# Kernel optimization log

Measured on AMD Instinct MI355X. Metric: run time of the kernel, lower is better.

## Reference

```python
import jax, jax.numpy as jnp
import numpy as np

B, N, IN_DIM, OUT_DIM, HEADS = 4, 2048, 128, 32, 8
NEG_SLOPE = 0.2


def setup_inputs() -> dict:
    key = jax.random.key(0)
    k_x, k_adj, k_w, k_as, k_ad = jax.random.split(key, 5)
    x = jax.random.normal(k_x, (B, N, IN_DIM), dtype=jnp.float32)
    adj = jax.random.randint(k_adj, (B, N, N), 0, 2).astype(jnp.float32)
    # xavier_uniform bounds
    lim_w = float(np.sqrt(6.0 / (IN_DIM + OUT_DIM)))
    lim_a = float(np.sqrt(6.0 / (OUT_DIM + 1)))
    W = jax.random.uniform(k_w, (HEADS, IN_DIM, OUT_DIM), dtype=jnp.float32, minval=-lim_w, maxval=lim_w)
    a_src = jax.random.uniform(k_as, (HEADS, OUT_DIM), dtype=jnp.float32, minval=-lim_a, maxval=lim_a)
    a_dst = jax.random.uniform(k_ad, (HEADS, OUT_DIM), dtype=jnp.float32, minval=-lim_a, maxval=lim_a)
    return {"x": x, "adj": adj, "W": W, "a_src": a_src, "a_dst": a_dst}


def reference(x, adj, W, a_src, a_dst):
    # Wh: [B,H,N,O]
    Wh = jnp.einsum('bnf,hfo->bhno', x, W)
    alpha_src = jnp.einsum('bhno,ho->bhn', Wh, a_src)  # [B,H,N]
    alpha_dst = jnp.einsum('bhno,ho->bhn', Wh, a_dst)  # [B,H,N]
    # additive scores e[b,h,i,j] = alpha_src[b,h,i] + alpha_dst[b,h,j]
    e = alpha_src[..., :, None] + alpha_dst[..., None, :]
    e = jnp.where(e >= 0, e, NEG_SLOPE * e)  # leaky_relu(0.2)
    n = adj.shape[-1]
    eye = jnp.eye(n, dtype=adj.dtype)
    mask = (adj + eye[None] > 0)[:, None, :, :]  # [B,1,N,N]
    e = jnp.where(mask, e, -jnp.inf)
    attn = jax.nn.softmax(e, axis=-1)  # every row has self-loop -> finite
    out = jnp.einsum('bhij,bhjo->bhio', attn, Wh)  # [B,H,N,O]
    b = x.shape[0]
    out = jnp.transpose(out, (0, 2, 1, 3)).reshape(b, n, HEADS * OUT_DIM)
    return jax.nn.relu(out)
```

## Files before the change

### kernel.cpp

```cpp
#include <hip/hip_runtime.h>
#include <math.h>

#define BB 4
#define NSZ 2048
#define FDIM 128
#define ODIM 32
#define HH 8

typedef short short8 __attribute__((ext_vector_type(8)));
typedef float f32x4 __attribute__((ext_vector_type(4)));

#define WS_EAP  0
#define WS_EBP  131072
#define WS_ADJB 262144
#define WS_WHF  786432
#define WS_WF   1835008

__device__ __forceinline__ unsigned bfbits(float f) {
    unsigned u = __builtin_bit_cast(unsigned, f);
    return u + 0x7fffu + ((u >> 16) & 1u);
}
__device__ __forceinline__ unsigned bfpack(float a, float b) {
    return __builtin_amdgcn_perm(bfbits(b), bfbits(a), 0x07060302);
}

__global__ __launch_bounds__(256) void k_wpack(const float* __restrict__ W,
                                               int4* __restrict__ wf) {
    int h = blockIdx.x;
    int t = threadIdx.x;
    int kt = t >> 6, lane = t & 63;
    int col = lane & 15, quad = lane >> 4;
    const float* wp = W + ((size_t)h * FDIM + kt * 32 + quad * 8) * ODIM;
#pragma unroll
    for (int ot = 0; ot < 2; ot++) {
        unsigned d[4];
#pragma unroll
        for (int jp = 0; jp < 4; jp++) {
            float lo = wp[(2 * jp) * ODIM + ot * 16 + col];
            float hi = wp[(2 * jp + 1) * ODIM + ot * 16 + col];
            d[jp] = bfpack(lo, hi);
        }
        wf[((h * 4 + kt) * 2 + ot) * 64 + lane] =
            make_int4((int)d[0], (int)d[1], (int)d[2], (int)d[3]);
    }
}

__global__ __launch_bounds__(256) void k_prep(const float* __restrict__ x,
                                              const float* __restrict__ adj,
                                              const float* __restrict__ a_src,
                                              const float* __restrict__ a_dst,
                                              const int4* __restrict__ wf,
                                              unsigned* __restrict__ adjb,
                                              int4* __restrict__ whf,
                                              float2* __restrict__ eap,
                                              float2* __restrict__ ebp) {
    __shared__ unsigned short wlds[64][33];
    int t = threadIdx.x;

    if (blockIdx.x < 16384) {
        int g = blockIdx.x * 256 + t;
        int l = g & 7;
        int word = g >> 3;
        int wk = word & 63;
        int row = word >> 6;
        int i = row & (NSZ - 1);
        const float4 v = *(const float4*)&adj[(size_t)row * NSZ + wk * 32 + l * 4];
        unsigned m = 0;
        if (v.x > 0.f) m |= 1u << (l * 4 + 0);
        if (v.y > 0.f) m |= 1u << (l * 4 + 1);
        if (v.z > 0.f) m |= 1u << (l * 4 + 2);
        if (v.w > 0.f) m |= 1u << (l * 4 + 3);
        m |= (unsigned)__shfl_xor((int)m, 1);
        m |= (unsigned)__shfl_xor((int)m, 2);
        m |= (unsigned)__shfl_xor((int)m, 4);
        if (l == 0) {
            int jb = i - wk * 32;
            if (jb >= 0 && jb < 32) m |= 1u << jb;
            adjb[word] = m;
        }
        return;
    }

    int bidx = blockIdx.x - 16384;
    int b = bidx >> 8;
    int h = (bidx >> 5) & 7;
    int nt = bidx & 31;
    int n0 = nt * 64;
    int w = t >> 6, lane = t & 63;
    int col = lane & 15, quad = lane >> 4;

    const float* xp = x + ((size_t)(b * NSZ) + n0 + w * 16 + col) * FDIM + quad * 8;
    int4 afr[4];
#pragma unroll
    for (int kt = 0; kt < 4; kt++) {
        float4 xa = *(const float4*)(xp + kt * 32);
        float4 xb = *(const float4*)(xp + kt * 32 + 4);
        afr[kt] = make_int4((int)bfpack(xa.x, xa.y), (int)bfpack(xa.z, xa.w),
                            (int)bfpack(xb.x, xb.y), (int)bfpack(xb.z, xb.w));
    }

    const int4* wfp = wf + h * 8 * 64 + lane;
    f32x4 alo = {0.f, 0.f, 0.f, 0.f};
    f32x4 ahi = {0.f, 0.f, 0.f, 0.f};
#pragma unroll
    for (int kt = 0; kt < 4; kt++) {
        short8 a8 = __builtin_bit_cast(short8, afr[kt]);
        alo = __builtin_amdgcn_mfma_f32_16x16x32_bf16(a8,
                __builtin_bit_cast(short8, wfp[(kt * 2 + 0) * 64]), alo, 0, 0, 0);
        ahi = __builtin_amdgcn_mfma_f32_16x16x32_bf16(a8,
                __builtin_bit_cast(short8, wfp[(kt * 2 + 1) * 64]), ahi, 0, 0, 0);
    }

    float as0 = a_src[h * ODIM + col], as1 = a_src[h * ODIM + 16 + col];
    float ad0 = a_dst[h * ODIM + col], ad1 = a_dst[h * ODIM + 16 + col];
#pragma unroll
    for (int r = 0; r < 4; r++) {
        float pa = alo[r] * as0 + ahi[r] * as1;
        float pb = alo[r] * ad0 + ahi[r] * ad1;
#pragma unroll
        for (int mk = 1; mk <= 8; mk <<= 1) {
            pa += __shfl_xor(pa, mk);
            pb += __shfl_xor(pb, mk);
        }
        if (col == 0) {
            size_t idx = (size_t)(b * HH + h) * NSZ + n0 + w * 16 + quad * 4 + r;
            eap[idx] = make_float2(__expf(pa - 8.f), __expf(0.2f * pa - 8.f));
            ebp[idx] = make_float2(__expf(pb - 8.f), __expf(0.2f * pb - 8.f));
        }
    }

#pragma unroll
    for (int r = 0; r < 4; r++) {
        wlds[w * 16 + quad * 4 + r][col]      = (unsigned short)(bfbits(alo[r]) >> 16);
        wlds[w * 16 + quad * 4 + r][col + 16] = (unsigned short)(bfbits(ahi[r]) >> 16);
    }
    __syncthreads();
    int jl = w >> 1, ot = w & 1;
    unsigned d[4];
#pragma unroll
    for (int jp = 0; jp < 4; jp++) {
        unsigned lo = wlds[jl * 32 + quad * 8 + 2 * jp][ot * 16 + col];
        unsigned hi = wlds[jl * 32 + quad * 8 + 2 * jp + 1][ot * 16 + col];
        d[jp] = (hi << 16) | lo;
    }
    int fragid = ((b * HH + h) * 64 + nt * 2 + jl) * 2 + ot;
    whf[(size_t)fragid * 64 + lane] = make_int4((int)d[0], (int)d[1], (int)d[2], (int)d[3]);
}

__device__ __forceinline__ int4 pfrag(float eaa, float eab, const float4& l0,
                                      const float4& l1, const float4& l2,
                                      const float4& l3, unsigned w) {
    float p0 = fmaxf(eaa * l0.x, eab * l0.y);
    float p1 = fmaxf(eaa * l0.z, eab * l0.w);
    float p2 = fmaxf(eaa * l1.x, eab * l1.y);
    float p3 = fmaxf(eaa * l1.z, eab * l1.w);
    float p4 = fmaxf(eaa * l2.x, eab * l2.y);
    float p5 = fmaxf(eaa * l2.z, eab * l2.w);
    float p6 = fmaxf(eaa * l3.x, eab * l3.y);
    float p7 = fmaxf(eaa * l3.z, eab * l3.w);
    p0 = (w & 1u)   ? p0 : 0.f;
    p1 = (w & 2u)   ? p1 : 0.f;
    p2 = (w & 4u)   ? p2 : 0.f;
    p3 = (w & 8u)   ? p3 : 0.f;
    p4 = (w & 16u)  ? p4 : 0.f;
    p5 = (w & 32u)  ? p5 : 0.f;
    p6 = (w & 64u)  ? p6 : 0.f;
    p7 = (w & 128u) ? p7 : 0.f;
    unsigned u0 = __builtin_bit_cast(unsigned, p0) + 0x8000u;
    unsigned u1 = __builtin_bit_cast(unsigned, p1) + 0x8000u;
    unsigned u2 = __builtin_bit_cast(unsigned, p2) + 0x8000u;
    unsigned u3 = __builtin_bit_cast(unsigned, p3) + 0x8000u;
    unsigned u4 = __builtin_bit_cast(unsigned, p4) + 0x8000u;
    unsigned u5 = __builtin_bit_cast(unsigned, p5) + 0x8000u;
    unsigned u6 = __builtin_bit_cast(unsigned, p6) + 0x8000u;
    unsigned u7 = __builtin_bit_cast(unsigned, p7) + 0x8000u;
    return make_int4((int)__builtin_amdgcn_perm(u1, u0, 0x07060302),
                     (int)__builtin_amdgcn_perm(u3, u2, 0x07060302),
                     (int)__builtin_amdgcn_perm(u5, u4, 0x07060302),
                     (int)__builtin_amdgcn_perm(u7, u6, 0x07060302));
}

__global__ __launch_bounds__(256) void k_gat(const int4* __restrict__ whf,
                                             const float2* __restrict__ eap,
                                             const float2* __restrict__ ebp,
                                             const unsigned* __restrict__ adjb,
                                             float* __restrict__ out) {
    __shared__ float ebl[4096];
    __shared__ float comb[2][24][64];

    int t = threadIdx.x;
    int u = blockIdx.x;
    int unit = (u & 7) * 128 + (u >> 3);
    int b = unit >> 8;
    int h = (unit >> 5) & 7;
    int i0 = (unit & 31) * 64;
    int wave = t >> 6, lane = t & 63;
    int it = wave & 1, jh = wave >> 1;
    int col = lane & 15, quad = lane >> 4, qsh = quad * 8;
    size_t bh = (size_t)(b * HH + h);

    const float4* ebg = (const float4*)(ebp + bh * NSZ);
#pragma unroll
    for (int k = 0; k < 4; k++) ((float4*)ebl)[t + k * 256] = ebg[t + k * 256];

    int iw = i0 + it * 32;
    float2 ea0 = eap[bh * NSZ + iw + col];
    float2 ea1 = eap[bh * NSZ + iw + 16 + col];
    const uint4* mp0 = (const uint4*)(adjb + ((size_t)(b * NSZ) + iw + col) * 64) + jh * 8;
    const uint4* mp1 = (const uint4*)(adjb + ((size_t)(b * NSZ) + iw + 16 + col) * 64) + jh * 8;
    const int4* bfp = whf + bh * 8192 + lane;

    f32x4 a00 = {0.f,0.f,0.f,0.f}, a01 = {0.f,0.f,0.f,0.f}, a0d = {0.f,0.f,0.f,0.f};
    f32x4 a10 = {0.f,0.f,0.f,0.f}, a11 = {0.f,0.f,0.f,0.f}, a1d = {0.f,0.f,0.f,0.f};
    const int4 onesv = make_int4(0x3F803F80, 0x3F803F80, 0x3F803F80, 0x3F803F80);
    short8 bones = __builtin_bit_cast(short8, onesv);

    __syncthreads();

    for (int jt4 = 0; jt4 < 8; jt4++) {
        uint4 m0 = mp0[jt4];
        uint4 m1 = mp1[jt4];
        unsigned m0a[4] = {m0.x, m0.y, m0.z, m0.w};
        unsigned m1a[4] = {m1.x, m1.y, m1.z, m1.w};
#pragma unroll
        for (int q = 0; q < 4; q++) {
            int jt = jh * 32 + jt4 * 4 + q;
            const float4* el = (const float4*)&ebl[(jt * 32 + qsh) * 2];
            float4 l0 = el[0], l1 = el[1], l2 = el[2], l3 = el[3];
            int4 blo = bfp[jt * 128];
            int4 bhi = bfp[jt * 128 + 64];
            int4 f0 = pfrag(ea0.x, ea0.y, l0, l1, l2, l3, m0a[q] >> qsh);
            int4 f1 = pfrag(ea1.x, ea1.y, l0, l1, l2, l3, m1a[q] >> qsh);
            short8 af0 = __builtin_bit_cast(short8, f0);
            short8 af1 = __builtin_bit_cast(short8, f1);
            short8 b0 = __builtin_bit_cast(short8, blo);
            short8 b1 = __builtin_bit_cast(short8, bhi);
            a00 = __builtin_amdgcn_mfma_f32_16x16x32_bf16(af0, b0, a00, 0, 0, 0);
            a01 = __builtin_amdgcn_mfma_f32_16x16x32_bf16(af0, b1, a01, 0, 0, 0);
            a0d = __builtin_amdgcn_mfma_f32_16x16x32_bf16(af0, bones, a0d, 0, 0, 0);
            a10 = __builtin_amdgcn_mfma_f32_16x16x32_bf16(af1, b0, a10, 0, 0, 0);
            a11 = __builtin_amdgcn_mfma_f32_16x16x32_bf16(af1, b1, a11, 0, 0, 0);
            a1d = __builtin_amdgcn_mfma_f32_16x16x32_bf16(af1, bones, a1d, 0, 0, 0);
        }
    }

    if (jh) {
#pragma unroll
        for (int r = 0; r < 4; r++) {
            comb[it][r][lane]      = a00[r];
            comb[it][4 + r][lane]  = a01[r];
            comb[it][8 + r][lane]  = a0d[r];
            comb[it][12 + r][lane] = a10[r];
            comb[it][16 + r][lane] = a11[r];
            comb[it][20 + r][lane] = a1d[r];
        }
    }
    __syncthreads();
    if (jh) return;
#pragma unroll
    for (int r = 0; r < 4; r++) {
        a00[r] += comb[it][r][lane];
        a01[r] += comb[it][4 + r][lane];
        a0d[r] += comb[it][8 + r][lane];
        a10[r] += comb[it][12 + r][lane];
        a11[r] += comb[it][16 + r][lane];
        a1d[r] += comb[it][20 + r][lane];
    }

    float* op = out + ((size_t)(b * NSZ) + iw) * (HH * ODIM) + h * ODIM + col;
#pragma unroll
    for (int r = 0; r < 4; r++) {
        int row = quad * 4 + r;
        float inv0 = 1.0f / a0d[r];
        float inv1 = 1.0f / a1d[r];
        op[(size_t)row * (HH * ODIM)]           = fmaxf(a00[r] * inv0, 0.f);
        op[(size_t)row * (HH * ODIM) + 16]      = fmaxf(a01[r] * inv0, 0.f);
        op[(size_t)(row + 16) * (HH * ODIM)]      = fmaxf(a10[r] * inv1, 0.f);
        op[(size_t)(row + 16) * (HH * ODIM) + 16] = fmaxf(a11[r] * inv1, 0.f);
    }
}

extern "C" void kernel_launch(void* const* d_in, const int* in_sizes, int n_in,
                              void* d_out, int out_size, void* d_ws, size_t ws_size,
                              hipStream_t stream) {
    const float* x     = (const float*)d_in[0];
    const float* adj   = (const float*)d_in[1];
    const float* W     = (const float*)d_in[2];
    const float* a_src = (const float*)d_in[3];
    const float* a_dst = (const float*)d_in[4];
    float* out = (float*)d_out;

    float* ws = (float*)d_ws;
    float2* eap    = (float2*)(ws + WS_EAP);
    float2* ebp    = (float2*)(ws + WS_EBP);
    unsigned* adjb = (unsigned*)(ws + WS_ADJB);
    int4* whf      = (int4*)(ws + WS_WHF);
    int4* wfr      = (int4*)(ws + WS_WF);

    k_wpack<<<dim3(HH), dim3(256), 0, stream>>>(W, wfr);
    k_prep<<<dim3(16384 + 1024), dim3(256), 0, stream>>>(x, adj, a_src, a_dst, wfr,
                                                         adjb, whf, eap, ebp);
    k_gat<<<dim3(BB * HH * (NSZ / 64)), dim3(256), 0, stream>>>(whf, eap, ebp, adjb, out);
}
```

Measured before the change: 147.5 us.

## Fuse W packing into prep kernel and mask P fragments via LDS lookup table

Removes the separate k_wpack launch. Each projection block of k_prep now stages its head's W slice in padded shared memory and builds the bf16 B fragments on the fly. In the attention kernel, the eight per-element select-by-bit masks are replaced with AND operations against a 16-entry LDS lookup table of 16-bit masks, applied after bf16 packing. This trades a kernel launch and some VALU selects for extra LDS traffic, per-block W loads, and a larger shared-memory footprint in k_prep.

```diff
diff --git a/kernel.cpp b/kernel.cpp
--- a/kernel.cpp
+++ b/kernel.cpp
@@ -14,7 +14,6 @@
 #define WS_EBP  131072
 #define WS_ADJB 262144
 #define WS_WHF  786432
-#define WS_WF   1835008
 
 __device__ __forceinline__ unsigned bfbits(float f) {
     unsigned u = __builtin_bit_cast(unsigned, f);
@@ -24,36 +23,16 @@
     return __builtin_amdgcn_perm(bfbits(b), bfbits(a), 0x07060302);
 }
 
-__global__ __launch_bounds__(256) void k_wpack(const float* __restrict__ W,
-                                               int4* __restrict__ wf) {
-    int h = blockIdx.x;
-    int t = threadIdx.x;
-    int kt = t >> 6, lane = t & 63;
-    int col = lane & 15, quad = lane >> 4;
-    const float* wp = W + ((size_t)h * FDIM + kt * 32 + quad * 8) * ODIM;
-#pragma unroll
-    for (int ot = 0; ot < 2; ot++) {
-        unsigned d[4];
-#pragma unroll
-        for (int jp = 0; jp < 4; jp++) {
-            float lo = wp[(2 * jp) * ODIM + ot * 16 + col];
-            float hi = wp[(2 * jp + 1) * ODIM + ot * 16 + col];
-            d[jp] = bfpack(lo, hi);
-        }
-        wf[((h * 4 + kt) * 2 + ot) * 64 + lane] =
-            make_int4((int)d[0], (int)d[1], (int)d[2], (int)d[3]);
-    }
-}
-
 __global__ __launch_bounds__(256) void k_prep(const float* __restrict__ x,
                                               const float* __restrict__ adj,
+                                              const float* __restrict__ W,
                                               const float* __restrict__ a_src,
                                               const float* __restrict__ a_dst,
-                                              const int4* __restrict__ wf,
                                               unsigned* __restrict__ adjb,
                                               int4* __restrict__ whf,
                                               float2* __restrict__ eap,
                                               float2* __restrict__ ebp) {
+    __shared__ float wsl[FDIM * 33];
     __shared__ unsigned short wlds[64][33];
     int t = threadIdx.x;
 
@@ -89,6 +68,12 @@
     int w = t >> 6, lane = t & 63;
     int col = lane & 15, quad = lane >> 4;
 
+#pragma unroll
+    for (int m = 0; m < 16; m++) {
+        int idx = t + m * 256;
+        wsl[(idx >> 5) * 33 + (idx & 31)] = W[(size_t)h * (FDIM * ODIM) + idx];
+    }
+
     const float* xp = x + ((size_t)(b * NSZ) + n0 + w * 16 + col) * FDIM + quad * 8;
     int4 afr[4];
 #pragma unroll
@@ -98,17 +83,30 @@
         afr[kt] = make_int4((int)bfpack(xa.x, xa.y), (int)bfpack(xa.z, xa.w),
                             (int)bfpack(xb.x, xb.y), (int)bfpack(xb.z, xb.w));
     }
-
-    const int4* wfp = wf + h * 8 * 64 + lane;
+    __syncthreads();
+
     f32x4 alo = {0.f, 0.f, 0.f, 0.f};
     f32x4 ahi = {0.f, 0.f, 0.f, 0.f};
 #pragma unroll
     for (int kt = 0; kt < 4; kt++) {
         short8 a8 = __builtin_bit_cast(short8, afr[kt]);
-        alo = __builtin_amdgcn_mfma_f32_16x16x32_bf16(a8,
-                __builtin_bit_cast(short8, wfp[(kt * 2 + 0) * 64]), alo, 0, 0, 0);
-        ahi = __builtin_amdgcn_mfma_f32_16x16x32_bf16(a8,
-                __builtin_bit_cast(short8, wfp[(kt * 2 + 1) * 64]), ahi, 0, 0, 0);
+#pragma unroll
+        for (int ot = 0; ot < 2; ot++) {
+            unsigned d[4];
+#pragma unroll
+            for (int jp = 0; jp < 4; jp++) {
+                float lo = wsl[(kt * 32 + quad * 8 + 2 * jp) * 33 + ot * 16 + col];
+                float hi = wsl[(kt * 32 + quad * 8 + 2 * jp + 1) * 33 + ot * 16 + col];
+                d[jp] = bfpack(lo, hi);
+            }
+            int4 bf = make_int4((int)d[0], (int)d[1], (int)d[2], (int)d[3]);
+            if (ot == 0)
+                alo = __builtin_amdgcn_mfma_f32_16x16x32_bf16(a8,
+                        __builtin_bit_cast(short8, bf), alo, 0, 0, 0);
+            else
+                ahi = __builtin_amdgcn_mfma_f32_16x16x32_bf16(a8,
+                        __builtin_bit_cast(short8, bf), ahi, 0, 0, 0);
+        }
     }
 
     float as0 = a_src[h * ODIM + col], as1 = a_src[h * ODIM + 16 + col];
@@ -149,7 +147,8 @@
 
 __device__ __forceinline__ int4 pfrag(float eaa, float eab, const float4& l0,
                                       const float4& l1, const float4& l2,
-                                      const float4& l3, unsigned w) {
+                                      const float4& l3, unsigned w,
+                                      const unsigned (*__restrict__ mlut)[2]) {
     float p0 = fmaxf(eaa * l0.x, eab * l0.y);
     float p1 = fmaxf(eaa * l0.z, eab * l0.w);
     float p2 = fmaxf(eaa * l1.x, eab * l1.y);
@@ -158,14 +157,6 @@
     float p5 = fmaxf(eaa * l2.z, eab * l2.w);
     float p6 = fmaxf(eaa * l3.x, eab * l3.y);
     float p7 = fmaxf(eaa * l3.z, eab * l3.w);
-    p0 = (w & 1u)   ? p0 : 0.f;
-    p1 = (w & 2u)   ? p1 : 0.f;
-    p2 = (w & 4u)   ? p2 : 0.f;
-    p3 = (w & 8u)   ? p3 : 0.f;
-    p4 = (w & 16u)  ? p4 : 0.f;
-    p5 = (w & 32u)  ? p5 : 0.f;
-    p6 = (w & 64u)  ? p6 : 0.f;
-    p7 = (w & 128u) ? p7 : 0.f;
     unsigned u0 = __builtin_bit_cast(unsigned, p0) + 0x8000u;
     unsigned u1 = __builtin_bit_cast(unsigned, p1) + 0x8000u;
     unsigned u2 = __builtin_bit_cast(unsigned, p2) + 0x8000u;
@@ -174,10 +165,14 @@
     unsigned u5 = __builtin_bit_cast(unsigned, p5) + 0x8000u;
     unsigned u6 = __builtin_bit_cast(unsigned, p6) + 0x8000u;
     unsigned u7 = __builtin_bit_cast(unsigned, p7) + 0x8000u;
-    return make_int4((int)__builtin_amdgcn_perm(u1, u0, 0x07060302),
-                     (int)__builtin_amdgcn_perm(u3, u2, 0x07060302),
-                     (int)__builtin_amdgcn_perm(u5, u4, 0x07060302),
-                     (int)__builtin_amdgcn_perm(u7, u6, 0x07060302));
+    unsigned d0 = __builtin_amdgcn_perm(u1, u0, 0x07060302);
+    unsigned d1 = __builtin_amdgcn_perm(u3, u2, 0x07060302);
+    unsigned d2 = __builtin_amdgcn_perm(u5, u4, 0x07060302);
+    unsigned d3 = __builtin_amdgcn_perm(u7, u6, 0x07060302);
+    const unsigned* mA = mlut[w & 15];
+    const unsigned* mB = mlut[(w >> 4) & 15];
+    return make_int4((int)(d0 & mA[0]), (int)(d1 & mA[1]),
+                     (int)(d2 & mB[0]), (int)(d3 & mB[1]));
 }
 
 __global__ __launch_bounds__(256) void k_gat(const int4* __restrict__ whf,
@@ -187,6 +182,7 @@
                                              float* __restrict__ out) {
     __shared__ float ebl[4096];
     __shared__ float comb[2][24][64];
+    __shared__ unsigned mlut[16][2];
 
     int t = threadIdx.x;
     int u = blockIdx.x;
@@ -199,6 +195,11 @@
     int col = lane & 15, quad = lane >> 4, qsh = quad * 8;
     size_t bh = (size_t)(b * HH + h);
 
+    if (t < 16) {
+        mlut[t][0] = ((t & 1) ? 0x0000FFFFu : 0u) | ((t & 2) ? 0xFFFF0000u : 0u);
+        mlut[t][1] = ((t & 4) ? 0x0000FFFFu : 0u) | ((t & 8) ? 0xFFFF0000u : 0u);
+    }
+
     const float4* ebg = (const float4*)(ebp + bh * NSZ);
 #pragma unroll
     for (int k = 0; k < 4; k++) ((float4*)ebl)[t + k * 256] = ebg[t + k * 256];
@@ -229,8 +230,8 @@
             float4 l0 = el[0], l1 = el[1], l2 = el[2], l3 = el[3];
             int4 blo = bfp[jt * 128];
             int4 bhi = bfp[jt * 128 + 64];
-            int4 f0 = pfrag(ea0.x, ea0.y, l0, l1, l2, l3, m0a[q] >> qsh);
-            int4 f1 = pfrag(ea1.x, ea1.y, l0, l1, l2, l3, m1a[q] >> qsh);
+            int4 f0 = pfrag(ea0.x, ea0.y, l0, l1, l2, l3, m0a[q] >> qsh, mlut);
+            int4 f1 = pfrag(ea1.x, ea1.y, l0, l1, l2, l3, m1a[q] >> qsh, mlut);
             short8 af0 = __builtin_bit_cast(short8, f0);
             short8 af1 = __builtin_bit_cast(short8, f1);
             short8 b0 = __builtin_bit_cast(short8, blo);
@@ -295,10 +296,8 @@
     float2* ebp    = (float2*)(ws + WS_EBP);
     unsigned* adjb = (unsigned*)(ws + WS_ADJB);
     int4* whf      = (int4*)(ws + WS_WHF);
-    int4* wfr      = (int4*)(ws + WS_WF);
-
-    k_wpack<<<dim3(HH), dim3(256), 0, stream>>>(W, wfr);
-    k_prep<<<dim3(16384 + 1024), dim3(256), 0, stream>>>(x, adj, a_src, a_dst, wfr,
+
+    k_prep<<<dim3(16384 + 1024), dim3(256), 0, stream>>>(x, adj, W, a_src, a_dst,
                                                          adjb, whf, eap, ebp);
     k_gat<<<dim3(BB * HH * (NSZ / 64)), dim3(256), 0, stream>>>(whf, eap, ebp, adjb, out);
 }
```

Measured after the change: 137.2 us, median of 2. 7.0% less time.
